# Optimization experiments

Measured on AMD Instinct MI355X. Metric: run time of the kernel, lower is better.

## Reference

```python
import jax, jax.numpy as jnp
import numpy as np

B, T, D, H, STEPS = 4096, 128, 4, 64, 60


def setup_inputs() -> dict:
    key = jax.random.key(0)
    ks = jax.random.split(key, 12)
    s = 0.1
    return {
        "x": jax.random.normal(ks[0], (B, T, D), dtype=jnp.float32),
        # layer 0 (input size D)
        "Wih0": jax.random.normal(ks[1], (4 * H, D), dtype=jnp.float32) * s,
        "Whh0": jax.random.normal(ks[2], (4 * H, H), dtype=jnp.float32) * s,
        "bih0": jax.random.normal(ks[3], (4 * H,), dtype=jnp.float32) * s,
        "bhh0": jax.random.normal(ks[4], (4 * H,), dtype=jnp.float32) * s,
        # layer 1 (input size H)
        "Wih1": jax.random.normal(ks[5], (4 * H, H), dtype=jnp.float32) * s,
        "Whh1": jax.random.normal(ks[6], (4 * H, H), dtype=jnp.float32) * s,
        "bih1": jax.random.normal(ks[7], (4 * H,), dtype=jnp.float32) * s,
        "bhh1": jax.random.normal(ks[8], (4 * H,), dtype=jnp.float32) * s,
        # output head
        "Wfc": jax.random.normal(ks[9], (D, H), dtype=jnp.float32) * s,
        "bfc": jax.random.normal(ks[10], (D,), dtype=jnp.float32) * s,
    }


def _lstm_cell(h, c, x, Wih, Whh, bih, bhh):
    # PyTorch gate order: i, f, g, o
    gates = x @ Wih.T + h @ Whh.T + (bih + bhh)  # [B, 4H]
    i, f, g, o = jnp.split(gates, 4, axis=-1)
    c_new = jax.nn.sigmoid(f) * c + jax.nn.sigmoid(i) * jnp.tanh(g)
    h_new = jax.nn.sigmoid(o) * jnp.tanh(c_new)
    return h_new, c_new


def reference(x, Wih0, Whh0, bih0, bhh0, Wih1, Whh1, bih1, bhh1, Wfc, bfc):
    b = x.shape[0]
    zeros = jnp.zeros((b, H), dtype=x.dtype)

    def two_layer(carry, xt):
        h0, c0, h1, c1 = carry
        h0, c0 = _lstm_cell(h0, c0, xt, Wih0, Whh0, bih0, bhh0)
        h1, c1 = _lstm_cell(h1, c1, h0, Wih1, Whh1, bih1, bhh1)
        return (h0, c0, h1, c1), h1

    # encode history: scan over time (xs: [T, B, D])
    carry0 = (zeros, zeros, zeros, zeros)
    carry, _ = jax.lax.scan(two_layer, carry0, jnp.swapaxes(x, 0, 1))

    def ar_step(state, _):
        carry, cur = state
        carry, h1 = two_layer(carry, cur)
        pred = h1 @ Wfc.T + bfc  # [B, D]
        return (carry, pred), pred

    _, preds = jax.lax.scan(ar_step, (carry, x[:, -1, :]), None, length=STEPS)
    return jnp.swapaxes(preds, 0, 1)  # [B, STEPS, D]
```

## Files before the change

kernel.cpp:

```cpp
#include <hip/hip_runtime.h>


#define T_ENC 128
#define D_IN 4
#define H 64
#define STEPS 60
#define M 16
#define A0S 104
#define A1S 136
#define XN (M * T_ENC * D_IN)
#define NT 512

typedef _Float16 half8 __attribute__((ext_vector_type(8)));
typedef _Float16 half4_t __attribute__((ext_vector_type(4)));
typedef float float4v __attribute__((ext_vector_type(4)));

__device__ __forceinline__ float fast_sigmoid(float x) {
    float e = __builtin_amdgcn_exp2f(-1.44269504f * x);
    return __builtin_amdgcn_rcpf(1.0f + e);
}
__device__ __forceinline__ float fast_tanh(float x) {
    float e = __builtin_amdgcn_exp2f(2.88539008f * x);
    return __builtin_fmaf(-2.0f, __builtin_amdgcn_rcpf(e + 1.0f), 1.0f);
}

__global__ __launch_bounds__(NT, 2) void lstm_ar_kernel(
    const float* __restrict__ x,
    const float* __restrict__ Wih0, const float* __restrict__ Whh0,
    const float* __restrict__ bih0, const float* __restrict__ bhh0,
    const float* __restrict__ Wih1, const float* __restrict__ Whh1,
    const float* __restrict__ bih1, const float* __restrict__ bhh1,
    const float* __restrict__ Wfc,  const float* __restrict__ bfc,
    float* __restrict__ out)
{
    __shared__ __align__(16) _Float16 A0buf[2][M * A0S];
    __shared__ __align__(16) _Float16 A1buf[2][M * A1S];
    __shared__ __align__(16) _Float16 xAll[XN];
    __shared__ __align__(16) float    predsS[M * STEPS * D_IN];

    const int tid   = threadIdx.x;
    const int wave  = tid >> 6;
    const int lane  = tid & 63;
    const int n16   = lane & 15;
    const int quad  = lane >> 4;
    const int w4    = wave & 3;
    const int whalf = wave >> 2;
    const int rbase = whalf * 2;
    const int m0    = blockIdx.x * M;
    const int m     = n16;
    const int jcol  = 16 * w4 + n16;

    { _Float16* z = &A0buf[0][0]; for (int i = tid; i < 2 * M * A0S; i += NT) z[i] = (_Float16)0.f; }
    { _Float16* z = &A1buf[0][0]; for (int i = tid; i < 2 * M * A1S; i += NT) z[i] = (_Float16)0.f; }
    for (int j = tid; j < XN / 4; j += NT) {
        const float4v v = *(const float4v*)&x[(size_t)m0 * T_ENC * D_IN + (size_t)j * 4];
        *(half4_t*)&xAll[j * 4] =
            (half4_t){(_Float16)v[0], (_Float16)v[1], (_Float16)v[2], (_Float16)v[3]};
    }

    half8 B1f[4][4];
    half8 BW0[4][4];
    float b1v[4], b0v[4], b0arv[4];
    #pragma unroll
    for (int tau = 0; tau < 4; ++tau) {
        const int n = 16 * (w4 + 4 * tau) + n16;
        b1v[tau] = bih1[n] + bhh1[n];
        b0v[tau] = bih0[n] + bhh0[n];
        float wb = 0.f;
        #pragma unroll
        for (int d = 0; d < 4; ++d) wb += Wih0[n * D_IN + d] * bfc[d];
        b0arv[tau] = b0v[tau] + wb;
        #pragma unroll
        for (int kt = 0; kt < 4; ++kt)
            #pragma unroll
            for (int j = 0; j < 8; ++j) {
                const int k = kt * 32 + quad * 8 + j;
                B1f[kt][tau][j] = (_Float16)((k < H) ? Wih1[n * H + k] : Whh1[n * H + (k - H)]);
                float v = 0.f;
                if (k < 4)       v = Wih0[n * D_IN + k];
                else if (k < 68) v = Whh0[n * H + (k - 4)];
                BW0[kt][tau][j] = (_Float16)v;
            }
    }
    half8 Bfc[2];
    float bfcv = 0.f;
    if (w4 == 0) {
        #pragma unroll
        for (int kt = 0; kt < 2; ++kt)
            #pragma unroll
            for (int j = 0; j < 8; ++j) {
                const int k = kt * 32 + quad * 8 + j;
                Bfc[kt][j] = (_Float16)((n16 < 4) ? Wfc[n16 * H + k] : 0.f);
            }
        if (n16 < 4) bfcv = bfc[n16];
    }

    float c0s[2] = {0.f, 0.f};
    float c1s[2] = {0.f, 0.f};

    __syncthreads();

    if (w4 == 2 && whalf == 0 && lane < 16) {
        *(half4_t*)&A0buf[1][lane * A0S] = *(const half4_t*)&xAll[(lane * T_ENC + 0) * D_IN];
        *(half4_t*)&A0buf[0][lane * A0S] = *(const half4_t*)&xAll[(lane * T_ENC + 1) * D_IN];
    }
    __syncthreads();

    {
        half8 a0f[3];
        #pragma unroll
        for (int kt = 0; kt < 3; ++kt)
            a0f[kt] = *(const half8*)&A0buf[1][m * A0S + kt * 32 + quad * 8];
        float4v C0[4];
        #pragma unroll
        for (int tau = 0; tau < 4; ++tau)
            C0[tau] = (float4v){b0v[tau], b0v[tau], b0v[tau], b0v[tau]};
        #pragma unroll
        for (int kt = 0; kt < 3; ++kt)
            #pragma unroll
            for (int tau = 0; tau < 4; ++tau)
                C0[tau] = __builtin_amdgcn_mfma_f32_16x16x32_f16(a0f[kt], BW0[kt][tau], C0[tau], 0, 0, 0);
        #pragma unroll
        for (int rr = 0; rr < 2; ++rr) {
            const int r = rbase + rr;
            const float ig = fast_sigmoid(C0[0][r]);
            const float fg = fast_sigmoid(C0[1][r]);
            const float gg = fast_tanh   (C0[2][r]);
            const float og = fast_sigmoid(C0[3][r]);
            const float c  = fg * c0s[rr] + ig * gg;
            c0s[rr] = c;
            const _Float16 hh = (_Float16)(og * fast_tanh(c));
            const int row = quad * 4 + r;
            A1buf[0][row * A1S + jcol]     = hh;
            A0buf[0][row * A0S + 4 + jcol] = hh;
        }
    }
    __syncthreads();

    for (int t = 0; t < T_ENC; ++t) {
        const int p = t & 1;
        const _Float16* cur0 = &A0buf[p][0];
        const _Float16* cur1 = &A1buf[p][0];
        _Float16* nxt0 = &A0buf[1 - p][0];
        _Float16* nxt1 = &A1buf[1 - p][0];

        half8 a1f[4], a0f[3];
        #pragma unroll
        for (int kt = 0; kt < 4; ++kt)
            a1f[kt] = *(const half8*)&cur1[m * A1S + kt * 32 + quad * 8];
        #pragma unroll
        for (int kt = 0; kt < 3; ++kt)
            a0f[kt] = *(const half8*)&cur0[m * A0S + kt * 32 + quad * 8];

        float4v C1[4], C0[4];
        #pragma unroll
        for (int tau = 0; tau < 4; ++tau) {
            C1[tau] = (float4v){b1v[tau], b1v[tau], b1v[tau], b1v[tau]};
            C0[tau] = (float4v){b0v[tau], b0v[tau], b0v[tau], b0v[tau]};
        }
        #pragma unroll
        for (int kt = 0; kt < 4; ++kt)
            #pragma unroll
            for (int tau = 0; tau < 4; ++tau)
                C1[tau] = __builtin_amdgcn_mfma_f32_16x16x32_f16(a1f[kt], B1f[kt][tau], C1[tau], 0, 0, 0);
        #pragma unroll
        for (int kt = 0; kt < 3; ++kt)
            #pragma unroll
            for (int tau = 0; tau < 4; ++tau)
                C0[tau] = __builtin_amdgcn_mfma_f32_16x16x32_f16(a0f[kt], BW0[kt][tau], C0[tau], 0, 0, 0);

        #pragma unroll
        for (int rr = 0; rr < 2; ++rr) {
            const int r = rbase + rr;
            const float ig = fast_sigmoid(C1[0][r]);
            const float fg = fast_sigmoid(C1[1][r]);
            const float gg = fast_tanh   (C1[2][r]);
            const float og = fast_sigmoid(C1[3][r]);
            const float c  = fg * c1s[rr] + ig * gg;
            c1s[rr] = c;
            nxt1[(quad * 4 + r) * A1S + 64 + jcol] = (_Float16)(og * fast_tanh(c));
        }
        #pragma unroll
        for (int rr = 0; rr < 2; ++rr) {
            const int r = rbase + rr;
            const float ig = fast_sigmoid(C0[0][r]);
            const float fg = fast_sigmoid(C0[1][r]);
            const float gg = fast_tanh   (C0[2][r]);
            const float og = fast_sigmoid(C0[3][r]);
            const float c  = fg * c0s[rr] + ig * gg;
            c0s[rr] = c;
            const _Float16 hh = (_Float16)(og * fast_tanh(c));
            const int row = quad * 4 + r;
            nxt1[row * A1S + jcol]     = hh;
            nxt0[row * A0S + 4 + jcol] = hh;
        }
        if (w4 == 2 && whalf == 0 && lane < 16) {
            int tn = t + 2; if (tn > T_ENC - 1) tn = T_ENC - 1;
            *(half4_t*)&nxt0[lane * A0S] = *(const half4_t*)&xAll[(lane * T_ENC + tn) * D_IN];
        }
        __syncthreads();
    }

    #pragma unroll
    for (int tau = 0; tau < 4; ++tau) {
        const int n = 16 * (w4 + 4 * tau) + n16;
        #pragma unroll
        for (int kt = 0; kt < 4; ++kt)
            #pragma unroll
            for (int j = 0; j < 8; ++j) {
                const int k = kt * 32 + quad * 8 + j;
                float v;
                if (k < H) v = Whh0[n * H + k];
                else {
                    const int c = k - H;
                    v = Wih0[n * D_IN + 0] * Wfc[0 * H + c] + Wih0[n * D_IN + 1] * Wfc[1 * H + c]
                      + Wih0[n * D_IN + 2] * Wfc[2 * H + c] + Wih0[n * D_IN + 3] * Wfc[3 * H + c];
                }
                BW0[kt][tau][j] = (_Float16)v;
            }
    }

    for (int s = 0; s < STEPS; ++s) {
        const int q = s & 1;
        const _Float16* cur = &A1buf[q][0];
        _Float16* nxt = &A1buf[1 - q][0];

        half8 a1f[4];
        #pragma unroll
        for (int kt = 0; kt < 4; ++kt)
            a1f[kt] = *(const half8*)&cur[m * A1S + kt * 32 + quad * 8];
        float4v C1[4];
        #pragma unroll
        for (int tau = 0; tau < 4; ++tau)
            C1[tau] = (float4v){b1v[tau], b1v[tau], b1v[tau], b1v[tau]};
        #pragma unroll
        for (int kt = 0; kt < 4; ++kt)
            #pragma unroll
            for (int tau = 0; tau < 4; ++tau)
                C1[tau] = __builtin_amdgcn_mfma_f32_16x16x32_f16(a1f[kt], B1f[kt][tau], C1[tau], 0, 0, 0);
        #pragma unroll
        for (int rr = 0; rr < 2; ++rr) {
            const int r = rbase + rr;
            const float ig = fast_sigmoid(C1[0][r]);
            const float fg = fast_sigmoid(C1[1][r]);
            const float gg = fast_tanh   (C1[2][r]);
            const float og = fast_sigmoid(C1[3][r]);
            const float c  = fg * c1s[rr] + ig * gg;
            c1s[rr] = c;
            nxt[(quad * 4 + r) * A1S + 64 + jcol] = (_Float16)(og * fast_tanh(c));
        }
        __syncthreads();

        half8 aA[4];
        #pragma unroll
        for (int kt = 0; kt < 2; ++kt)
            aA[kt] = *(const half8*)&cur[m * A1S + kt * 32 + quad * 8];
        #pragma unroll
        for (int kt = 0; kt < 2; ++kt)
            aA[2 + kt] = *(const half8*)&nxt[m * A1S + 64 + kt * 32 + quad * 8];
        float4v C0[4];
        #pragma unroll
        for (int tau = 0; tau < 4; ++tau)
            C0[tau] = (float4v){b0arv[tau], b0arv[tau], b0arv[tau], b0arv[tau]};
        #pragma unroll
        for (int kt = 0; kt < 4; ++kt)
            #pragma unroll
            for (int tau = 0; tau < 4; ++tau)
                C0[tau] = __builtin_amdgcn_mfma_f32_16x16x32_f16(aA[kt], BW0[kt][tau], C0[tau], 0, 0, 0);

        if (w4 == 0) {
            float4v Cp = (float4v){bfcv, bfcv, bfcv, bfcv};
            Cp = __builtin_amdgcn_mfma_f32_16x16x32_f16(aA[2], Bfc[0], Cp, 0, 0, 0);
            Cp = __builtin_amdgcn_mfma_f32_16x16x32_f16(aA[3], Bfc[1], Cp, 0, 0, 0);
            if (n16 < 4) {
                #pragma unroll
                for (int rr = 0; rr < 2; ++rr) {
                    const int r = rbase + rr;
                    predsS[(quad * 4 + r) * (STEPS * D_IN) + s * D_IN + n16] = Cp[r];
                }
            }
        }

        #pragma unroll
        for (int rr = 0; rr < 2; ++rr) {
            const int r = rbase + rr;
            const float ig = fast_sigmoid(C0[0][r]);
            const float fg = fast_sigmoid(C0[1][r]);
            const float gg = fast_tanh   (C0[2][r]);
            const float og = fast_sigmoid(C0[3][r]);
            const float c  = fg * c0s[rr] + ig * gg;
            c0s[rr] = c;
            nxt[(quad * 4 + r) * A1S + jcol] = (_Float16)(og * fast_tanh(c));
        }
        __syncthreads();
    }

    for (int j = tid; j < M * STEPS; j += NT) {
        const int elem = j / STEPS, r = j - elem * STEPS;
        ((float4v*)out)[(size_t)(m0 + elem) * STEPS + r] = ((const float4v*)predsS)[j];
    }
}

extern "C" void kernel_launch(void* const* d_in, const int* in_sizes, int n_in,
                              void* d_out, int out_size, void* d_ws, size_t ws_size,
                              hipStream_t stream) {
    const float* x    = (const float*)d_in[0];
    const float* Wih0 = (const float*)d_in[1];
    const float* Whh0 = (const float*)d_in[2];
    const float* bih0 = (const float*)d_in[3];
    const float* bhh0 = (const float*)d_in[4];
    const float* Wih1 = (const float*)d_in[5];
    const float* Whh1 = (const float*)d_in[6];
    const float* bih1 = (const float*)d_in[7];
    const float* bhh1 = (const float*)d_in[8];
    const float* Wfc  = (const float*)d_in[9];
    const float* bfc  = (const float*)d_in[10];
    float* out = (float*)d_out;

    dim3 grid(4096 / M);
    dim3 block(NT);
    lstm_ar_kernel<<<grid, block, 0, stream>>>(
        x, Wih0, Whh0, bih0, bhh0, Wih1, Whh1, bih1, bhh1, Wfc, bfc, out);
}
```

Measured before the change: 326.9 us.

## Split batch into 8-row blocks of four waves and drop the half-wave row split

Each block now owns 8 batch rows instead of 16, runs 256 threads instead of 512, and the grid doubles. Each wave now applies the gate nonlinearities to all four accumulator rows, where before two wave halves each took two rows after running the same MFMAs. The goal is more independent blocks per CU, so one block's barrier stalls can be hidden by another block's work. The cost is that the 16-row MFMA tiles are now half padding and each wave does twice the scalar gate work per step.

```diff
diff --git a/kernel.cpp b/kernel.cpp
--- a/kernel.cpp
+++ b/kernel.cpp
@@ -5,11 +5,11 @@
 #define D_IN 4
 #define H 64
 #define STEPS 60
-#define M 16
+#define MR 8
 #define A0S 104
 #define A1S 136
-#define XN (M * T_ENC * D_IN)
-#define NT 512
+#define XN (MR * T_ENC * D_IN)
+#define NT 256
 
 typedef _Float16 half8 __attribute__((ext_vector_type(8)));
 typedef _Float16 half4_t __attribute__((ext_vector_type(4)));
@@ -33,25 +33,22 @@
     const float* __restrict__ Wfc,  const float* __restrict__ bfc,
     float* __restrict__ out)
 {
-    __shared__ __align__(16) _Float16 A0buf[2][M * A0S];
-    __shared__ __align__(16) _Float16 A1buf[2][M * A1S];
+    __shared__ __align__(16) _Float16 A0buf[2][16 * A0S];
+    __shared__ __align__(16) _Float16 A1buf[2][16 * A1S];
     __shared__ __align__(16) _Float16 xAll[XN];
-    __shared__ __align__(16) float    predsS[M * STEPS * D_IN];
-
-    const int tid   = threadIdx.x;
-    const int wave  = tid >> 6;
-    const int lane  = tid & 63;
-    const int n16   = lane & 15;
-    const int quad  = lane >> 4;
-    const int w4    = wave & 3;
-    const int whalf = wave >> 2;
-    const int rbase = whalf * 2;
-    const int m0    = blockIdx.x * M;
-    const int m     = n16;
-    const int jcol  = 16 * w4 + n16;
-
-    { _Float16* z = &A0buf[0][0]; for (int i = tid; i < 2 * M * A0S; i += NT) z[i] = (_Float16)0.f; }
-    { _Float16* z = &A1buf[0][0]; for (int i = tid; i < 2 * M * A1S; i += NT) z[i] = (_Float16)0.f; }
+    __shared__ __align__(16) float    predsS[MR * STEPS * D_IN];
+
+    const int tid  = threadIdx.x;
+    const int wave = tid >> 6;
+    const int lane = tid & 63;
+    const int n16  = lane & 15;
+    const int quad = lane >> 4;
+    const int m0   = blockIdx.x * MR;
+    const int m    = n16;
+    const int jcol = 16 * wave + n16;
+
+    { _Float16* z = &A0buf[0][0]; for (int i = tid; i < 2 * 16 * A0S; i += NT) z[i] = (_Float16)0.f; }
+    { _Float16* z = &A1buf[0][0]; for (int i = tid; i < 2 * 16 * A1S; i += NT) z[i] = (_Float16)0.f; }
     for (int j = tid; j < XN / 4; j += NT) {
         const float4v v = *(const float4v*)&x[(size_t)m0 * T_ENC * D_IN + (size_t)j * 4];
         *(half4_t*)&xAll[j * 4] =
@@ -63,7 +60,7 @@
     float b1v[4], b0v[4], b0arv[4];
     #pragma unroll
     for (int tau = 0; tau < 4; ++tau) {
-        const int n = 16 * (w4 + 4 * tau) + n16;
+        const int n = 16 * (wave + 4 * tau) + n16;
         b1v[tau] = bih1[n] + bhh1[n];
         b0v[tau] = bih0[n] + bhh0[n];
         float wb = 0.f;
@@ -84,7 +81,7 @@
     }
     half8 Bfc[2];
     float bfcv = 0.f;
-    if (w4 == 0) {
+    if (wave == 0) {
         #pragma unroll
         for (int kt = 0; kt < 2; ++kt)
             #pragma unroll
@@ -95,12 +92,12 @@
         if (n16 < 4) bfcv = bfc[n16];
     }
 
-    float c0s[2] = {0.f, 0.f};
-    float c1s[2] = {0.f, 0.f};
+    float c0s[4] = {0.f, 0.f, 0.f, 0.f};
+    float c1s[4] = {0.f, 0.f, 0.f, 0.f};
 
     __syncthreads();
 
-    if (w4 == 2 && whalf == 0 && lane < 16) {
+    if (wave == 2 && lane < MR) {
         *(half4_t*)&A0buf[1][lane * A0S] = *(const half4_t*)&xAll[(lane * T_ENC + 0) * D_IN];
         *(half4_t*)&A0buf[0][lane * A0S] = *(const half4_t*)&xAll[(lane * T_ENC + 1) * D_IN];
     }
@@ -121,14 +118,13 @@
             for (int tau = 0; tau < 4; ++tau)
                 C0[tau] = __builtin_amdgcn_mfma_f32_16x16x32_f16(a0f[kt], BW0[kt][tau], C0[tau], 0, 0, 0);
         #pragma unroll
-        for (int rr = 0; rr < 2; ++rr) {
-            const int r = rbase + rr;
+        for (int r = 0; r < 4; ++r) {
             const float ig = fast_sigmoid(C0[0][r]);
             const float fg = fast_sigmoid(C0[1][r]);
             const float gg = fast_tanh   (C0[2][r]);
             const float og = fast_sigmoid(C0[3][r]);
-            const float c  = fg * c0s[rr] + ig * gg;
-            c0s[rr] = c;
+            const float c  = fg * c0s[r] + ig * gg;
+            c0s[r] = c;
             const _Float16 hh = (_Float16)(og * fast_tanh(c));
             const int row = quad * 4 + r;
             A1buf[0][row * A1S + jcol]     = hh;
@@ -170,31 +166,29 @@
                 C0[tau] = __builtin_amdgcn_mfma_f32_16x16x32_f16(a0f[kt], BW0[kt][tau], C0[tau], 0, 0, 0);
 
         #pragma unroll
-        for (int rr = 0; rr < 2; ++rr) {
-            const int r = rbase + rr;
+        for (int r = 0; r < 4; ++r) {
             const float ig = fast_sigmoid(C1[0][r]);
             const float fg = fast_sigmoid(C1[1][r]);
             const float gg = fast_tanh   (C1[2][r]);
             const float og = fast_sigmoid(C1[3][r]);
-            const float c  = fg * c1s[rr] + ig * gg;
-            c1s[rr] = c;
+            const float c  = fg * c1s[r] + ig * gg;
+            c1s[r] = c;
             nxt1[(quad * 4 + r) * A1S + 64 + jcol] = (_Float16)(og * fast_tanh(c));
         }
         #pragma unroll
-        for (int rr = 0; rr < 2; ++rr) {
-            const int r = rbase + rr;
+        for (int r = 0; r < 4; ++r) {
             const float ig = fast_sigmoid(C0[0][r]);
             const float fg = fast_sigmoid(C0[1][r]);
             const float gg = fast_tanh   (C0[2][r]);
             const float og = fast_sigmoid(C0[3][r]);
-            const float c  = fg * c0s[rr] + ig * gg;
-            c0s[rr] = c;
+            const float c  = fg * c0s[r] + ig * gg;
+            c0s[r] = c;
             const _Float16 hh = (_Float16)(og * fast_tanh(c));
             const int row = quad * 4 + r;
             nxt1[row * A1S + jcol]     = hh;
             nxt0[row * A0S + 4 + jcol] = hh;
         }
-        if (w4 == 2 && whalf == 0 && lane < 16) {
+        if (wave == 2 && lane < MR) {
             int tn = t + 2; if (tn > T_ENC - 1) tn = T_ENC - 1;
             *(half4_t*)&nxt0[lane * A0S] = *(const half4_t*)&xAll[(lane * T_ENC + tn) * D_IN];
         }
@@ -203,7 +197,7 @@
 
     #pragma unroll
     for (int tau = 0; tau < 4; ++tau) {
-        const int n = 16 * (w4 + 4 * tau) + n16;
+        const int n = 16 * (wave + 4 * tau) + n16;
         #pragma unroll
         for (int kt = 0; kt < 4; ++kt)
             #pragma unroll
@@ -239,14 +233,13 @@
             for (int tau = 0; tau < 4; ++tau)
                 C1[tau] = __builtin_amdgcn_mfma_f32_16x16x32_f16(a1f[kt], B1f[kt][tau], C1[tau], 0, 0, 0);
         #pragma unroll
-        for (int rr = 0; rr < 2; ++rr) {
-            const int r = rbase + rr;
+        for (int r = 0; r < 4; ++r) {
             const float ig = fast_sigmoid(C1[0][r]);
             const float fg = fast_sigmoid(C1[1][r]);
             const float gg = fast_tanh   (C1[2][r]);
             const float og = fast_sigmoid(C1[3][r]);
-            const float c  = fg * c1s[rr] + ig * gg;
-            c1s[rr] = c;
+            const float c  = fg * c1s[r] + ig * gg;
+            c1s[r] = c;
             nxt[(quad * 4 + r) * A1S + 64 + jcol] = (_Float16)(og * fast_tanh(c));
         }
         __syncthreads();
@@ -268,34 +261,31 @@
             for (int tau = 0; tau < 4; ++tau)
                 C0[tau] = __builtin_amdgcn_mfma_f32_16x16x32_f16(aA[kt], BW0[kt][tau], C0[tau], 0, 0, 0);
 
-        if (w4 == 0) {
+        if (wave == 0) {
             float4v Cp = (float4v){bfcv, bfcv, bfcv, bfcv};
             Cp = __builtin_amdgcn_mfma_f32_16x16x32_f16(aA[2], Bfc[0], Cp, 0, 0, 0);
             Cp = __builtin_amdgcn_mfma_f32_16x16x32_f16(aA[3], Bfc[1], Cp, 0, 0, 0);
-            if (n16 < 4) {
+            if (n16 < 4 && quad < MR / 4) {
                 #pragma unroll
-                for (int rr = 0; rr < 2; ++rr) {
-                    const int r = rbase + rr;
+                for (int r = 0; r < 4; ++r)
                     predsS[(quad * 4 + r) * (STEPS * D_IN) + s * D_IN + n16] = Cp[r];
-                }
             }
         }
 
         #pragma unroll
-        for (int rr = 0; rr < 2; ++rr) {
-            const int r = rbase + rr;
+        for (int r = 0; r < 4; ++r) {
             const float ig = fast_sigmoid(C0[0][r]);
             const float fg = fast_sigmoid(C0[1][r]);
             const float gg = fast_tanh   (C0[2][r]);
             const float og = fast_sigmoid(C0[3][r]);
-            const float c  = fg * c0s[rr] + ig * gg;
-            c0s[rr] = c;
+            const float c  = fg * c0s[r] + ig * gg;
+            c0s[r] = c;
             nxt[(quad * 4 + r) * A1S + jcol] = (_Float16)(og * fast_tanh(c));
         }
         __syncthreads();
     }
 
-    for (int j = tid; j < M * STEPS; j += NT) {
+    for (int j = tid; j < MR * STEPS; j += NT) {
         const int elem = j / STEPS, r = j - elem * STEPS;
         ((float4v*)out)[(size_t)(m0 + elem) * STEPS + r] = ((const float4v*)predsS)[j];
     }
@@ -317,7 +307,7 @@
     const float* bfc  = (const float*)d_in[10];
     float* out = (float*)d_out;
 
-    dim3 grid(4096 / M);
+    dim3 grid(4096 / MR);
     dim3 block(NT);
     lstm_ar_kernel<<<grid, block, 0, stream>>>(
         x, Wih0, Whh0, bih0, bhh0, Wih1, Whh1, bih1, bhh1, Wfc, bfc, out);
```

After: 379.6 us. 1.16x slower.
